# Kernel optimization log

Measured on AMD Instinct MI355X. Metric: run time of the kernel, lower is better.

## Reference

```python
import jax, jax.numpy as jnp
import numpy as np

HEADS = 16
HEAD_DIM = 128


def rotate_half(x):
    x1, x2 = x[..., : x.shape[-1] // 2], x[..., x.shape[-1] // 2 :]
    return jnp.concatenate((-x2, x1), axis=-1)


def setup_inputs() -> dict:
    key = jax.random.key(0)
    ks = jax.random.split(key, 8)
    b, s, h = 2, 2048, 2048
    d = HEAD_DIM
    sc = 1.0 / np.sqrt(h)
    x = jax.random.normal(ks[0], (b, s, h), jnp.float32)
    # real RoPE angles for realism
    inv_freq = 1.0 / (10000.0 ** (jnp.arange(0, d, 2, dtype=jnp.float32) / d))
    t = jnp.arange(s, dtype=jnp.float32)
    freqs = jnp.outer(t, inv_freq)  # [s, d/2]
    emb = jnp.concatenate((freqs, freqs), axis=-1)  # [s, d]
    return {
        "x": x,
        "cos": jnp.cos(emb),
        "sin": jnp.sin(emb),
        "wq": jax.random.normal(ks[1], (h, h), jnp.float32) * sc,
        "bq": jnp.zeros((h,), jnp.float32),
        "wk": jax.random.normal(ks[2], (h, h), jnp.float32) * sc,
        "bk": jnp.zeros((h,), jnp.float32),
        "wv": jax.random.normal(ks[3], (h, h), jnp.float32) * sc,
        "bv": jnp.zeros((h,), jnp.float32),
        "wo": jax.random.normal(ks[4], (h, h), jnp.float32) * sc,
    }


def reference(x, cos, sin, wq, bq, wk, bk, wv, bv, wo):
    b, s, hidden = x.shape
    nh, d = HEADS, HEAD_DIM
    # QKV projections (F.linear: x @ W.T + b)
    def split_heads(t):
        return t.reshape(b, s, nh, d).transpose(0, 2, 1, 3)  # [b,h,s,d]
    q = split_heads(x @ wq.T + bq)
    k = split_heads(x @ wk.T + bk)
    v = split_heads(x @ wv.T + bv)
    # RoPE (cos/sin: [s,d] broadcast over [b,h,s,d])
    q = q * cos + rotate_half(q) * sin
    k = k * cos + rotate_half(k) * sin
    # full (non-causal) attention, materializing [b,h,s,s] scores as original
    scale = 1.0 / jnp.sqrt(jnp.asarray(d, x.dtype))
    scores = jnp.einsum("bhqd,bhkd->bhqk", q, k) * scale
    attn = jax.nn.softmax(scores, axis=-1)
    out = jnp.einsum("bhqk,bhkd->bhqd", attn, v)  # [b,h,s,d]
    out = out.transpose(0, 2, 1, 3).reshape(b, s, hidden)
    # o_proj: no bias
    return out @ wo.T
```

## Files before the change

### kernel.cpp

```cpp
#include <hip/hip_runtime.h>

#define B_  2
#define NH  16
#define S_  2048
#define D_  128
#define HID 2048

typedef _Float16 half_t;
typedef _Float16 f16x8 __attribute__((ext_vector_type(8)));
typedef _Float16 f16x4_t __attribute__((ext_vector_type(4)));
typedef float f32x4 __attribute__((ext_vector_type(4)));

__device__ __forceinline__ void glds16(const half_t* g, half_t* l) {
    __builtin_amdgcn_global_load_lds(
        (const __attribute__((address_space(1))) void*)g,
        (__attribute__((address_space(3))) void*)l, 16, 0, 0);
}

__global__ __launch_bounds__(256) void cvt_all(
    const float* __restrict__ x,  const float* __restrict__ wq, const float* __restrict__ wk,
    const float* __restrict__ wv, const float* __restrict__ wo, half_t* __restrict__ dst)
{
    long i = ((long)blockIdx.x * 256 + threadIdx.x) * 4;
    const float* src; long off;
    if (i < 8388608)       { src = x;  off = i; }
    else if (i < 12582912) { src = wq; off = i - 8388608; }
    else if (i < 16777216) { src = wk; off = i - 12582912; }
    else if (i < 20971520) { src = wv; off = i - 16777216; }
    else                   { src = wo; off = i - 20971520; }
    float4 v = *(const float4*)(src + off);
    f16x4_t h;
    h[0] = (half_t)v.x; h[1] = (half_t)v.y; h[2] = (half_t)v.z; h[3] = (half_t)v.w;
    *(f16x4_t*)(dst + i) = h;
}

__global__ __launch_bounds__(256, 3) void qkv_gemm(
    const half_t* __restrict__ xb,
    const half_t* __restrict__ wqb, const half_t* __restrict__ wkb, const half_t* __restrict__ wvb,
    const float* __restrict__ bq, const float* __restrict__ bk, const float* __restrict__ bv,
    const float* __restrict__ cosp, const float* __restrict__ sinp,
    half_t* __restrict__ qo, half_t* __restrict__ ko, half_t* __restrict__ vto)
{
    __shared__ __align__(16) half_t As[128 * 32];
    __shared__ __align__(16) half_t Bs[128 * 32];
    const int m0 = blockIdx.x * 128;
    const int n0 = blockIdx.y * 128;
    const int z  = blockIdx.z;
    const half_t* wb   = (z == 0) ? wqb : (z == 1) ? wkb : wvb;
    const float*  bias = (z == 0) ? bq  : (z == 1) ? bk  : bv;
    const int tid = threadIdx.x, wave = tid >> 6, lane = tid & 63;
    const int quad = lane >> 4, lrow = lane & 15;
    const int wm = wave >> 1, wn = wave & 1;

    const int r0 = wave * 32 + (lane >> 2);
    const int r1 = r0 + 16;
    const int c0 = (((lane & 3) - (r0 >> 1)) & 3) * 8;
    const int c1 = (((lane & 3) - (r1 >> 1)) & 3) * 8;
    const half_t* ag0 = xb + (size_t)(m0 + r0) * HID + c0;
    const half_t* ag1 = xb + (size_t)(m0 + r1) * HID + c1;
    const half_t* bg0 = wb + (size_t)(n0 + r0) * HID + c0;
    const half_t* bg1 = wb + (size_t)(n0 + r1) * HID + c1;
    half_t* al0 = &As[(wave * 32) * 32];
    half_t* al1 = &As[(wave * 32 + 16) * 32];
    half_t* bl0 = &Bs[(wave * 32) * 32];
    half_t* bl1 = &Bs[(wave * 32 + 16) * 32];

    f32x4 acc[4][4] = {};

    for (int k0 = 0; k0 < HID; k0 += 32) {
        __syncthreads();
        glds16(ag0 + k0, al0);
        glds16(ag1 + k0, al1);
        glds16(bg0 + k0, bl0);
        glds16(bg1 + k0, bl1);
        __syncthreads();
        f16x8 af[4], bf[4];
#pragma unroll
        for (int mt = 0; mt < 4; mt++) {
            const int ra = wm * 64 + mt * 16 + lrow;
            const int pa = (quad + (ra >> 1)) & 3;
            af[mt] = *(const f16x8*)&As[ra * 32 + pa * 8];
        }
#pragma unroll
        for (int nt = 0; nt < 4; nt++) {
            const int rb = wn * 16 + nt * 32 + lrow;
            const int pb = (quad + (rb >> 1)) & 3;
            bf[nt] = *(const f16x8*)&Bs[rb * 32 + pb * 8];
        }
#pragma unroll
        for (int mt = 0; mt < 4; mt++)
#pragma unroll
            for (int nt = 0; nt < 4; nt++)
                acc[mt][nt] = __builtin_amdgcn_mfma_f32_16x16x32_f16(af[mt], bf[nt], acc[mt][nt], 0, 0, 0);
    }

    const int head = blockIdx.y;
    float bs_[4];
#pragma unroll
    for (int nt = 0; nt < 4; nt++) bs_[nt] = bias[n0 + nt * 32 + wn * 16 + lrow];
#pragma unroll
    for (int mt = 0; mt < 4; mt++) {
#pragma unroll
        for (int r = 0; r < 4; r++) {
            const int m  = m0 + wm * 64 + mt * 16 + quad * 4 + r;
            const int bb = m >> 11;
            const int st = m & (S_ - 1);
            float res[4];
#pragma unroll
            for (int nt = 0; nt < 4; nt++) res[nt] = acc[mt][nt][r] + bs_[nt];
            if (z < 2) {
                const float* cr = cosp + st * D_;
                const float* sr = sinp + st * D_;
#pragma unroll
                for (int pr = 0; pr < 2; pr++) {
                    const int dlo = pr * 32 + wn * 16 + lrow;
                    float cl = cr[dlo], sl = sr[dlo], ch = cr[dlo + 64], sh = sr[dlo + 64];
                    float lo = res[pr], hi = res[pr + 2];
                    res[pr]     = lo * cl - hi * sl;
                    res[pr + 2] = hi * ch + lo * sh;
                }
                half_t* dst = (z == 0 ? qo : ko) + ((size_t)(bb * NH + head) * S_ + st) * D_;
#pragma unroll
                for (int nt = 0; nt < 4; nt++) dst[nt * 32 + wn * 16 + lrow] = (half_t)res[nt];
            } else {
                half_t* dst = vto + (size_t)(bb * NH + head) * D_ * S_ + st;
#pragma unroll
                for (int nt = 0; nt < 4; nt++) dst[(size_t)(nt * 32 + wn * 16 + lrow) * S_] = (half_t)res[nt];
            }
        }
    }
}

#define PLD 72
__global__ __launch_bounds__(256, 3) void attn_kernel(
    const half_t* __restrict__ qb, const half_t* __restrict__ kb,
    const half_t* __restrict__ vtb, half_t* __restrict__ ob)
{
    __shared__ __align__(16) half_t ks[64 * 128];
    __shared__ __align__(16) half_t vs[128 * 64];
    __shared__ __align__(16) half_t ps[4 * 16 * PLD];
    const int head = blockIdx.y, b = blockIdx.z;
    const int bh = b * NH + head;
    const int tid = threadIdx.x, wave = tid >> 6, lane = tid & 63;
    const int quad = lane >> 4, lrow = lane & 15;
    const float scale = 0.08838834764831845f;
    const int q0 = blockIdx.x * 64 + wave * 16;

    f16x8 qf[4];
    {
        const half_t* qrow = qb + ((size_t)bh * S_ + q0 + lrow) * D_;
#pragma unroll
        for (int kc = 0; kc < 4; kc++) {
            f16x8 v = *(const f16x8*)(qrow + kc * 32 + quad * 8);
#pragma unroll
            for (int j = 0; j < 8; j++) v[j] = (half_t)((float)v[j] * scale);
            qf[kc] = v;
        }
    }

    const half_t* kbase = kb + (size_t)bh * S_ * D_;
    const half_t* vbase = vtb + (size_t)bh * D_ * S_;
    const int pbase = wave * 16 * PLD;

    float m_run[4], l_run[4];
#pragma unroll
    for (int r = 0; r < 4; r++) { m_run[r] = -1e30f; l_run[r] = 0.f; }
    f32x4 o[8] = {};

    for (int kt = 0; kt < 32; kt++) {
        __syncthreads();
#pragma unroll
        for (int i = 0; i < 4; i++) {
            const int rk = wave * 16 + i * 4 + (lane >> 4);
            const int ck = (((lane & 15) - (rk & 7)) & 15) * 8;
            glds16(kbase + (size_t)(kt * 64 + rk) * D_ + ck, &ks[(wave * 16 + i * 4) * 128]);
            const int rv = wave * 32 + i * 8 + (lane >> 3);
            const int cv = (((lane & 7) - (rv & 7)) & 7) * 8;
            glds16(vbase + (size_t)rv * S_ + kt * 64 + cv, &vs[(wave * 32 + i * 8) * 64]);
        }
        __syncthreads();

        f32x4 s[4] = {};
#pragma unroll
        for (int nt = 0; nt < 4; nt++) {
            const int rk2 = nt * 16 + lrow;
#pragma unroll
            for (int kc = 0; kc < 4; kc++) {
                const int pk = (kc * 4 + quad + (rk2 & 7)) & 15;
                f16x8 kf = *(const f16x8*)&ks[rk2 * 128 + pk * 8];
                s[nt] = __builtin_amdgcn_mfma_f32_16x16x32_f16(qf[kc], kf, s[nt], 0, 0, 0);
            }
        }

        float alpha_r[4];
        bool upd = false;
#pragma unroll
        for (int r = 0; r < 4; r++) {
            float mx = fmaxf(fmaxf(s[0][r], s[1][r]), fmaxf(s[2][r], s[3][r]));
#pragma unroll
            for (int off = 1; off < 16; off <<= 1) mx = fmaxf(mx, __shfl_xor(mx, off));
            const float mnew = fmaxf(m_run[r], mx);
            alpha_r[r] = __expf(m_run[r] - mnew);
            upd = upd || (mnew != m_run[r]);
            m_run[r] = mnew;
            float p0 = __expf(s[0][r] - mnew);
            float p1 = __expf(s[1][r] - mnew);
            float p2 = __expf(s[2][r] - mnew);
            float p3 = __expf(s[3][r] - mnew);
            float rs = (p0 + p1) + (p2 + p3);
#pragma unroll
            for (int off = 1; off < 16; off <<= 1) rs += __shfl_xor(rs, off);
            l_run[r] = l_run[r] * alpha_r[r] + rs;
            const int prow = pbase + (quad * 4 + r) * PLD + lrow;
            ps[prow]      = (half_t)p0;
            ps[prow + 16] = (half_t)p1;
            ps[prow + 32] = (half_t)p2;
            ps[prow + 48] = (half_t)p3;
        }
        if (__any(upd)) {
#pragma unroll
            for (int r = 0; r < 4; r++)
#pragma unroll
                for (int dt = 0; dt < 8; dt++) o[dt][r] *= alpha_r[r];
        }

#pragma unroll
        for (int kc2 = 0; kc2 < 2; kc2++) {
            f16x8 pf = *(const f16x8*)&ps[pbase + lrow * PLD + kc2 * 32 + quad * 8];
#pragma unroll
            for (int dt = 0; dt < 8; dt++) {
                const int rv2 = dt * 16 + lrow;
                const int pv = (kc2 * 4 + quad + (rv2 & 7)) & 7;
                f16x8 vf = *(const f16x8*)&vs[rv2 * 64 + pv * 8];
                o[dt] = __builtin_amdgcn_mfma_f32_16x16x32_f16(pf, vf, o[dt], 0, 0, 0);
            }
        }
    }

    float rl[4];
#pragma unroll
    for (int r = 0; r < 4; r++) rl[r] = 1.f / l_run[r];
#pragma unroll
    for (int dt = 0; dt < 8; dt++) {
        const int d = dt * 16 + lrow;
#pragma unroll
        for (int r = 0; r < 4; r++) {
            const int row = q0 + quad * 4 + r;
            ob[((size_t)b * S_ + row) * HID + head * D_ + d] = (half_t)(o[dt][r] * rl[r]);
        }
    }
}

__global__ __launch_bounds__(256, 3) void out_gemm(
    const half_t* __restrict__ ab, const half_t* __restrict__ wob, float* __restrict__ out)
{
    __shared__ __align__(16) half_t As[128 * 32];
    __shared__ __align__(16) half_t Bs[128 * 32];
    const int m0 = blockIdx.x * 128;
    const int n0 = blockIdx.y * 128;
    const int tid = threadIdx.x, wave = tid >> 6, lane = tid & 63;
    const int quad = lane >> 4, lrow = lane & 15;
    const int wm = wave >> 1, wn = wave & 1;

    const int r0 = wave * 32 + (lane >> 2);
    const int r1 = r0 + 16;
    const int c0 = (((lane & 3) - (r0 >> 1)) & 3) * 8;
    const int c1 = (((lane & 3) - (r1 >> 1)) & 3) * 8;
    const half_t* ag0 = ab  + (size_t)(m0 + r0) * HID + c0;
    const half_t* ag1 = ab  + (size_t)(m0 + r1) * HID + c1;
    const half_t* bg0 = wob + (size_t)(n0 + r0) * HID + c0;
    const half_t* bg1 = wob + (size_t)(n0 + r1) * HID + c1;
    half_t* al0 = &As[(wave * 32) * 32];
    half_t* al1 = &As[(wave * 32 + 16) * 32];
    half_t* bl0 = &Bs[(wave * 32) * 32];
    half_t* bl1 = &Bs[(wave * 32 + 16) * 32];

    f32x4 acc[4][4] = {};

    for (int k0 = 0; k0 < HID; k0 += 32) {
        __syncthreads();
        glds16(ag0 + k0, al0);
        glds16(ag1 + k0, al1);
        glds16(bg0 + k0, bl0);
        glds16(bg1 + k0, bl1);
        __syncthreads();
        f16x8 af[4], bf[4];
#pragma unroll
        for (int mt = 0; mt < 4; mt++) {
            const int ra = wm * 64 + mt * 16 + lrow;
            const int pa = (quad + (ra >> 1)) & 3;
            af[mt] = *(const f16x8*)&As[ra * 32 + pa * 8];
        }
#pragma unroll
        for (int nt = 0; nt < 4; nt++) {
            const int rb = wn * 16 + nt * 32 + lrow;
            const int pb = (quad + (rb >> 1)) & 3;
            bf[nt] = *(const f16x8*)&Bs[rb * 32 + pb * 8];
        }
#pragma unroll
        for (int mt = 0; mt < 4; mt++)
#pragma unroll
            for (int nt = 0; nt < 4; nt++)
                acc[mt][nt] = __builtin_amdgcn_mfma_f32_16x16x32_f16(af[mt], bf[nt], acc[mt][nt], 0, 0, 0);
    }

#pragma unroll
    for (int mt = 0; mt < 4; mt++)
#pragma unroll
        for (int r = 0; r < 4; r++) {
            const int m = m0 + wm * 64 + mt * 16 + quad * 4 + r;
#pragma unroll
            for (int nt = 0; nt < 4; nt++)
                out[(size_t)m * HID + n0 + nt * 32 + wn * 16 + lrow] = acc[mt][nt][r];
        }
}

extern "C" void kernel_launch(void* const* d_in, const int* in_sizes, int n_in,
                              void* d_out, int out_size, void* d_ws, size_t ws_size,
                              hipStream_t stream)
{
    const float* x    = (const float*)d_in[0];
    const float* cosp = (const float*)d_in[1];
    const float* sinp = (const float*)d_in[2];
    const float* wq   = (const float*)d_in[3];
    const float* bq   = (const float*)d_in[4];
    const float* wk   = (const float*)d_in[5];
    const float* bk   = (const float*)d_in[6];
    const float* wv   = (const float*)d_in[7];
    const float* bv   = (const float*)d_in[8];
    const float* wo   = (const float*)d_in[9];
    float* out = (float*)d_out;

    half_t* w   = (half_t*)d_ws;
    half_t* xb  = w;
    half_t* wqb = xb  + 8388608;
    half_t* wkb = wqb + 4194304;
    half_t* wvb = wkb + 4194304;
    half_t* wob = wvb + 4194304;
    half_t* qo  = wob + 4194304;
    half_t* ko  = qo  + 8388608;
    half_t* vto = ko  + 8388608;
    half_t* ob  = vto + 8388608;

    cvt_all<<<24576, 256, 0, stream>>>(x, wq, wk, wv, wo, xb);
    qkv_gemm<<<dim3(32, 16, 3), 256, 0, stream>>>(xb, wqb, wkb, wvb, bq, bk, bv,
                                                  cosp, sinp, qo, ko, vto);
    attn_kernel<<<dim3(32, 16, 2), 256, 0, stream>>>(qo, ko, vto, ob);
    out_gemm<<<dim3(32, 16), 256, 0, stream>>>(ob, wob, out);
}
```

Before: 493.7 us.

## Process 32 query rows per wave in attention and use exp2 softmax

Each attention wave now handles two 16-row query tiles, so every K/V tile staged in shared memory feeds twice as many MFMAs. The grid is halved, and the block count per SM hint drops from 3 to 2. Scores are computed transposed (K as the A operand), so the row max and row sum need only two cross-lane shuffles, and P is written to LDS as packed 4-element vectors. The scale is folded with log2(e) so softmax can use the hardware exp2. The cost is more registers and fewer blocks in flight, which lowers occupancy.

Measured after the change: 422.4 us. 1.17x faster.

```diff
diff --git a/kernel.cpp b/kernel.cpp
--- a/kernel.cpp
+++ b/kernel.cpp
@@ -16,6 +16,7 @@
         (const __attribute__((address_space(1))) void*)g,
         (__attribute__((address_space(3))) void*)l, 16, 0, 0);
 }
+__device__ __forceinline__ float fexp2(float x) { return __builtin_amdgcn_exp2f(x); }
 
 __global__ __launch_bounds__(256) void cvt_all(
     const float* __restrict__ x,  const float* __restrict__ wq, const float* __restrict__ wk,
@@ -132,40 +133,39 @@
 }
 
 #define PLD 72
-__global__ __launch_bounds__(256, 3) void attn_kernel(
+__global__ __launch_bounds__(256, 2) void attn_kernel(
     const half_t* __restrict__ qb, const half_t* __restrict__ kb,
     const half_t* __restrict__ vtb, half_t* __restrict__ ob)
 {
     __shared__ __align__(16) half_t ks[64 * 128];
     __shared__ __align__(16) half_t vs[128 * 64];
-    __shared__ __align__(16) half_t ps[4 * 16 * PLD];
+    __shared__ __align__(16) half_t ps[4 * 32 * PLD];
     const int head = blockIdx.y, b = blockIdx.z;
     const int bh = b * NH + head;
     const int tid = threadIdx.x, wave = tid >> 6, lane = tid & 63;
     const int quad = lane >> 4, lrow = lane & 15;
-    const float scale = 0.08838834764831845f;
-    const int q0 = blockIdx.x * 64 + wave * 16;
-
-    f16x8 qf[4];
-    {
-        const half_t* qrow = qb + ((size_t)bh * S_ + q0 + lrow) * D_;
+    const float SC = 0.08838834764831845f * 1.4426950408889634f;
+    const int q0 = blockIdx.x * 128 + wave * 32;
+
+    f16x8 qf[2][4];
+#pragma unroll
+    for (int mt = 0; mt < 2; mt++) {
+        const half_t* qrow = qb + ((size_t)bh * S_ + q0 + mt * 16 + lrow) * D_;
 #pragma unroll
         for (int kc = 0; kc < 4; kc++) {
             f16x8 v = *(const f16x8*)(qrow + kc * 32 + quad * 8);
 #pragma unroll
-            for (int j = 0; j < 8; j++) v[j] = (half_t)((float)v[j] * scale);
-            qf[kc] = v;
+            for (int j = 0; j < 8; j++) v[j] = (half_t)((float)v[j] * SC);
+            qf[mt][kc] = v;
         }
     }
 
     const half_t* kbase = kb + (size_t)bh * S_ * D_;
     const half_t* vbase = vtb + (size_t)bh * D_ * S_;
-    const int pbase = wave * 16 * PLD;
-
-    float m_run[4], l_run[4];
-#pragma unroll
-    for (int r = 0; r < 4; r++) { m_run[r] = -1e30f; l_run[r] = 0.f; }
-    f32x4 o[8] = {};
+    const int pbase = wave * 32 * PLD;
+
+    float m_run[2] = {-1e30f, -1e30f}, l_run[2] = {0.f, 0.f};
+    f32x4 o[2][8] = {};
 
     for (int kt = 0; kt < 32; kt++) {
         __syncthreads();
@@ -180,7 +180,7 @@
         }
         __syncthreads();
 
-        f32x4 s[4] = {};
+        f32x4 st[2][4] = {};
 #pragma unroll
         for (int nt = 0; nt < 4; nt++) {
             const int rk2 = nt * 16 + lrow;
@@ -188,65 +188,84 @@
             for (int kc = 0; kc < 4; kc++) {
                 const int pk = (kc * 4 + quad + (rk2 & 7)) & 15;
                 f16x8 kf = *(const f16x8*)&ks[rk2 * 128 + pk * 8];
-                s[nt] = __builtin_amdgcn_mfma_f32_16x16x32_f16(qf[kc], kf, s[nt], 0, 0, 0);
-            }
-        }
-
-        float alpha_r[4];
+                st[0][nt] = __builtin_amdgcn_mfma_f32_16x16x32_f16(kf, qf[0][kc], st[0][nt], 0, 0, 0);
+                st[1][nt] = __builtin_amdgcn_mfma_f32_16x16x32_f16(kf, qf[1][kc], st[1][nt], 0, 0, 0);
+            }
+        }
+
         bool upd = false;
-#pragma unroll
-        for (int r = 0; r < 4; r++) {
-            float mx = fmaxf(fmaxf(s[0][r], s[1][r]), fmaxf(s[2][r], s[3][r]));
-#pragma unroll
-            for (int off = 1; off < 16; off <<= 1) mx = fmaxf(mx, __shfl_xor(mx, off));
-            const float mnew = fmaxf(m_run[r], mx);
-            alpha_r[r] = __expf(m_run[r] - mnew);
-            upd = upd || (mnew != m_run[r]);
-            m_run[r] = mnew;
-            float p0 = __expf(s[0][r] - mnew);
-            float p1 = __expf(s[1][r] - mnew);
-            float p2 = __expf(s[2][r] - mnew);
-            float p3 = __expf(s[3][r] - mnew);
-            float rs = (p0 + p1) + (p2 + p3);
-#pragma unroll
-            for (int off = 1; off < 16; off <<= 1) rs += __shfl_xor(rs, off);
-            l_run[r] = l_run[r] * alpha_r[r] + rs;
-            const int prow = pbase + (quad * 4 + r) * PLD + lrow;
-            ps[prow]      = (half_t)p0;
-            ps[prow + 16] = (half_t)p1;
-            ps[prow + 32] = (half_t)p2;
-            ps[prow + 48] = (half_t)p3;
+        float alpha[2];
+#pragma unroll
+        for (int mt = 0; mt < 2; mt++) {
+            float m01 = fmaxf(fmaxf(st[mt][0][0], st[mt][0][1]), fmaxf(st[mt][0][2], st[mt][0][3]));
+            float m11 = fmaxf(fmaxf(st[mt][1][0], st[mt][1][1]), fmaxf(st[mt][1][2], st[mt][1][3]));
+            float m21 = fmaxf(fmaxf(st[mt][2][0], st[mt][2][1]), fmaxf(st[mt][2][2], st[mt][2][3]));
+            float m31 = fmaxf(fmaxf(st[mt][3][0], st[mt][3][1]), fmaxf(st[mt][3][2], st[mt][3][3]));
+            float mx = fmaxf(fmaxf(m01, m11), fmaxf(m21, m31));
+            mx = fmaxf(mx, __shfl_xor(mx, 16));
+            mx = fmaxf(mx, __shfl_xor(mx, 32));
+            const float mnew = fmaxf(m_run[mt], mx);
+            alpha[mt] = fexp2(m_run[mt] - mnew);
+            upd = upd || (mnew > m_run[mt]);
+            m_run[mt] = mnew;
+            float rs = 0.f;
+#pragma unroll
+            for (int nt = 0; nt < 4; nt++) {
+                f16x4_t pk4;
+#pragma unroll
+                for (int r = 0; r < 4; r++) {
+                    float p = fexp2(st[mt][nt][r] - mnew);
+                    rs += p;
+                    pk4[r] = (half_t)p;
+                }
+                *(f16x4_t*)&ps[pbase + (mt * 16 + lrow) * PLD + nt * 16 + quad * 4] = pk4;
+            }
+            rs += __shfl_xor(rs, 16);
+            rs += __shfl_xor(rs, 32);
+            l_run[mt] = l_run[mt] * alpha[mt] + rs;
         }
         if (__any(upd)) {
 #pragma unroll
-            for (int r = 0; r < 4; r++)
-#pragma unroll
-                for (int dt = 0; dt < 8; dt++) o[dt][r] *= alpha_r[r];
+            for (int mt = 0; mt < 2; mt++) {
+                float ab[4];
+#pragma unroll
+                for (int r = 0; r < 4; r++) ab[r] = __shfl(alpha[mt], quad * 4 + r, 16);
+#pragma unroll
+                for (int dt = 0; dt < 8; dt++)
+#pragma unroll
+                    for (int r = 0; r < 4; r++) o[mt][dt][r] *= ab[r];
+            }
         }
 
 #pragma unroll
         for (int kc2 = 0; kc2 < 2; kc2++) {
-            f16x8 pf = *(const f16x8*)&ps[pbase + lrow * PLD + kc2 * 32 + quad * 8];
+            f16x8 pf0 = *(const f16x8*)&ps[pbase + lrow * PLD + kc2 * 32 + quad * 8];
+            f16x8 pf1 = *(const f16x8*)&ps[pbase + (16 + lrow) * PLD + kc2 * 32 + quad * 8];
 #pragma unroll
             for (int dt = 0; dt < 8; dt++) {
                 const int rv2 = dt * 16 + lrow;
                 const int pv = (kc2 * 4 + quad + (rv2 & 7)) & 7;
                 f16x8 vf = *(const f16x8*)&vs[rv2 * 64 + pv * 8];
-                o[dt] = __builtin_amdgcn_mfma_f32_16x16x32_f16(pf, vf, o[dt], 0, 0, 0);
-            }
-        }
-    }
-
-    float rl[4];
-#pragma unroll
-    for (int r = 0; r < 4; r++) rl[r] = 1.f / l_run[r];
-#pragma unroll
-    for (int dt = 0; dt < 8; dt++) {
-        const int d = dt * 16 + lrow;
-#pragma unroll
-        for (int r = 0; r < 4; r++) {
-            const int row = q0 + quad * 4 + r;
-            ob[((size_t)b * S_ + row) * HID + head * D_ + d] = (half_t)(o[dt][r] * rl[r]);
+                o[0][dt] = __builtin_amdgcn_mfma_f32_16x16x32_f16(pf0, vf, o[0][dt], 0, 0, 0);
+                o[1][dt] = __builtin_amdgcn_mfma_f32_16x16x32_f16(pf1, vf, o[1][dt], 0, 0, 0);
+            }
+        }
+    }
+
+#pragma unroll
+    for (int mt = 0; mt < 2; mt++) {
+        const float rl = 1.f / l_run[mt];
+        float rb[4];
+#pragma unroll
+        for (int r = 0; r < 4; r++) rb[r] = __shfl(rl, quad * 4 + r, 16);
+#pragma unroll
+        for (int dt = 0; dt < 8; dt++) {
+            const int d = dt * 16 + lrow;
+#pragma unroll
+            for (int r = 0; r < 4; r++) {
+                const int row = q0 + mt * 16 + quad * 4 + r;
+                ob[((size_t)b * S_ + row) * HID + head * D_ + d] = (half_t)(o[mt][dt][r] * rb[r]);
+            }
         }
     }
 }
@@ -345,6 +364,6 @@
     cvt_all<<<24576, 256, 0, stream>>>(x, wq, wk, wv, wo, xb);
     qkv_gemm<<<dim3(32, 16, 3), 256, 0, stream>>>(xb, wqb, wkb, wvb, bq, bk, bv,
                                                   cosp, sinp, qo, ko, vto);
-    attn_kernel<<<dim3(32, 16, 2), 256, 0, stream>>>(qo, ko, vto, ob);
+    attn_kernel<<<dim3(16, 16, 2), 256, 0, stream>>>(qo, ko, vto, ob);
     out_gemm<<<dim3(32, 16), 256, 0, stream>>>(ob, wob, out);
 }
```
